# Kernel tuning notes

Measured on AMD Instinct MI355X. Metric: run time of the kernel, lower is better.

Reference implementation:

```python
import jax, jax.numpy as jnp
import numpy as np
import math

B, S, D, H, DK, DFF = 64, 512, 512, 8, 64, 2048


def _layernorm(x, g, b, eps=1e-5):
    mu = jnp.mean(x, axis=-1, keepdims=True)
    var = jnp.var(x, axis=-1, keepdims=True)
    return (x - mu) * jax.lax.rsqrt(var + eps) * g + b


def setup_inputs() -> dict:
    key = jax.random.key(0)
    ks = jax.random.split(key, 16)
    std = 0.02
    return {
        "query": jax.random.normal(ks[0], (B, S, D), jnp.float32),
        "key": jax.random.normal(ks[1], (B, S, D), jnp.float32),
        "values": jax.random.normal(ks[2], (B, S, D), jnp.float32),
        "forget_rate": jax.random.uniform(ks[3], (B, 1, S, 1), jnp.float32),
        "Wq": jax.random.normal(ks[4], (D, D), jnp.float32) * std,
        "bq": jnp.zeros((D,), jnp.float32),
        "Wk": jax.random.normal(ks[5], (D, D), jnp.float32) * std,
        "bk": jnp.zeros((D,), jnp.float32),
        "Wv": jax.random.normal(ks[6], (D, D), jnp.float32) * std,
        "bv": jnp.zeros((D,), jnp.float32),
        "Wo": jax.random.normal(ks[7], (D, D), jnp.float32) * std,
        "bo": jnp.zeros((D,), jnp.float32),
        "g1": jnp.ones((D,), jnp.float32),
        "beta1": jnp.zeros((D,), jnp.float32),
        "W1": jax.random.normal(ks[8], (D, DFF), jnp.float32) * std,
        "bf1": jnp.zeros((DFF,), jnp.float32),
        "W2": jax.random.normal(ks[9], (DFF, D), jnp.float32) * std,
        "bf2": jnp.zeros((D,), jnp.float32),
        "g2": jnp.ones((D,), jnp.float32),
        "beta2": jnp.zeros((D,), jnp.float32),
        "mask": 0,
    }


def reference(query, key, values, forget_rate, Wq, bq, Wk, bk, Wv, bv, Wo, bo,
              g1, beta1, W1, bf1, W2, bf2, g2, beta2, mask):
    bs, seqlen, _ = query.shape
    # project and split heads -> [B, H, S, DK]
    q = (query @ Wq + bq).reshape(bs, seqlen, H, DK).transpose(0, 2, 1, 3)
    k = (key @ Wk + bk).reshape(bs, seqlen, H, DK).transpose(0, 2, 1, 3)
    v = (values @ Wv + bv).reshape(bs, seqlen, H, DK).transpose(0, 2, 1, 3)

    scores = jnp.einsum('bhqd,bhkd->bhqk', q, k) / math.sqrt(DK)  # [B,H,S,S]
    # forget_rate [B,1,S,1] broadcasts over heads and key dim (== repeat in torch)
    scores = scores * forget_rate
    # src_mask: allowed where triu(ones, k=mask) == 0, i.e. j < i + mask
    allowed = jnp.tril(jnp.ones((seqlen, seqlen), bool), mask - 1)
    scores = jnp.where(allowed, scores, jnp.float32(-1e32))
    probs = jax.nn.softmax(scores, axis=-1)
    if mask == 0:  # zero_pad: overwrite first query row with zeros
        probs = probs.at[:, :, 0, :].set(0.0)
    out = jnp.einsum('bhqk,bhkd->bhqd', probs, v)  # [B,H,S,DK]
    concat = out.transpose(0, 2, 1, 3).reshape(bs, seqlen, D)
    attn_out = concat @ Wo + bo

    x = _layernorm(query + attn_out, g1, beta1)
    ff = jax.nn.relu(x @ W1 + bf1) @ W2 + bf2
    x = _layernorm(x + ff, g2, beta2)
    return x
```

## Files before the change

kernel.cpp:

```cpp
#include <hip/hip_runtime.h>
#include <hip/hip_bf16.h>
#include <stdint.h>

typedef __attribute__((ext_vector_type(8))) short short8;
typedef __attribute__((ext_vector_type(8))) unsigned short ushort8;
typedef __attribute__((ext_vector_type(4))) unsigned short ushort4v;
typedef __attribute__((ext_vector_type(4))) float f32x4;

#define DEV static __device__ __forceinline__

constexpr int Bc = 64, Sc = 512, Dc = 512, Hc = 8, DKc = 64, DFc = 2048;
constexpr int Mtot = Bc * Sc;
constexpr int CB   = 16;
constexpr int RC   = CB * Sc;
constexpr int RH   = 16384;

DEV unsigned short f2b(float f) {
    union { float f; unsigned u; } x; x.f = f;
    unsigned r = x.u + 0x7fffu + ((x.u >> 16) & 1u);
    return (unsigned short)(r >> 16);
}
DEV float b2f(unsigned short u) {
    union { unsigned u; float f; } x; x.u = ((unsigned)u) << 16; return x.f;
}

DEV void gload16(const void* g, void* l) {
    __builtin_amdgcn_global_load_lds(
        (const __attribute__((address_space(1))) void*)g,
        (__attribute__((address_space(3))) void*)l, 16, 0, 0);
}

__global__ void k_cvt(const float* __restrict__ in, unsigned short* __restrict__ out, int n8) {
    int idx = blockIdx.x * 256 + threadIdx.x;
    if (idx >= n8) return;
    const float4* p = (const float4*)(in + (size_t)idx * 8);
    float4 a = p[0], b = p[1];
    ushort8 o;
    o[0] = f2b(a.x); o[1] = f2b(a.y); o[2] = f2b(a.z); o[3] = f2b(a.w);
    o[4] = f2b(b.x); o[5] = f2b(b.y); o[6] = f2b(b.z); o[7] = f2b(b.w);
    *(ushort8*)(out + (size_t)idx * 8) = o;
}

__global__ void k_copy8(const unsigned short* __restrict__ in, unsigned short* __restrict__ out, int n8) {
    int idx = blockIdx.x * 256 + threadIdx.x;
    if (idx >= n8) return;
    *(ushort8*)(out + (size_t)idx * 8) = *(const ushort8*)(in + (size_t)idx * 8);
}

__global__ void k_cvt_w_all(
    const float* __restrict__ Wq, const float* __restrict__ Wk, const float* __restrict__ Wv,
    const float* __restrict__ Wo, const float* __restrict__ W1, const float* __restrict__ W2,
    unsigned short* __restrict__ Wqt, unsigned short* __restrict__ Wkt,
    unsigned short* __restrict__ Wvt, unsigned short* __restrict__ Wot,
    unsigned short* __restrict__ W1t, unsigned short* __restrict__ W2t) {
    int idx = blockIdx.x * 256 + threadIdx.x;
    const float* in; unsigned short* out; int K, N, li;
    if (idx < 131072) {
        int w = idx >> 15, r = idx & 32767;
        const float* ins[4] = {Wq, Wk, Wv, Wo};
        unsigned short* outs[4] = {Wqt, Wkt, Wvt, Wot};
        in = ins[w]; out = outs[w]; K = 512; N = 512; li = r;
    } else if (idx < 262144) {
        in = W1; out = W1t; K = 512; N = 2048; li = idx - 131072;
    } else {
        in = W2; out = W2t; K = 2048; N = 512; li = idx - 262144;
    }
    int kc = li % (K / 8), n = li / (K / 8);
    ushort8 o;
    #pragma unroll
    for (int j = 0; j < 8; ++j) o[j] = f2b(in[(size_t)(kc * 8 + j) * N + n]);
    *(ushort8*)(out + (size_t)n * K + kc * 8) = o;
}

template<int BM, int BN>
DEV void gemm_core(const unsigned short* __restrict__ A, int lda,
                   const unsigned short* __restrict__ Bt, int ldb, int K,
                   unsigned short* lA, unsigned short* lB,
                   f32x4 (&acc)[BM / 32][BN / 32]) {
    constexpr int MF = BM / 32, NF = BN / 32;
    const int tid = threadIdx.x, lane = tid & 63, wv = tid >> 6;
    const int wr = wv >> 1, wc = wv & 1;
    const int l15 = lane & 15, l4 = lane >> 4, l7 = l15 & 7;
    #pragma unroll
    for (int mf = 0; mf < MF; ++mf)
        #pragma unroll
        for (int nf = 0; nf < NF; ++nf)
            acc[mf][nf] = f32x4{0.f, 0.f, 0.f, 0.f};

    auto stage = [&](int buf, int kt0) {
        unsigned short* dA = lA + (size_t)buf * BM * 64;
        #pragma unroll
        for (int r = 0; r < BM / 32; ++r) {
            int c = r * 256 + tid, row = c >> 3, gs = c & 7;
            gload16(A + (size_t)row * lda + kt0 + ((gs ^ (row & 7)) * 8),
                    dA + (size_t)(r * 256 + wv * 64) * 8);
        }
        unsigned short* dB = lB + (size_t)buf * BN * 64;
        #pragma unroll
        for (int r = 0; r < BN / 32; ++r) {
            int c = r * 256 + tid, row = c >> 3, gs = c & 7;
            gload16(Bt + (size_t)row * ldb + kt0 + ((gs ^ (row & 7)) * 8),
                    dB + (size_t)(r * 256 + wv * 64) * 8);
        }
    };

    stage(0, 0);
    __syncthreads();
    const int nk = K / 64;
    for (int t = 0; t < nk; ++t) {
        const int buf = t & 1;
        if (t + 1 < nk) stage(buf ^ 1, (t + 1) * 64);
        const unsigned short* cA = lA + (size_t)buf * BM * 64;
        const unsigned short* cB = lB + (size_t)buf * BN * 64;
        #pragma unroll
        for (int kt = 0; kt < 2; ++kt) {
            short8 af[MF], bfr[NF];
            #pragma unroll
            for (int mf = 0; mf < MF; ++mf)
                af[mf] = *(const short8*)&cA[(wr * (BM / 2) + mf * 16 + l15) * 64 +
                                             (((kt * 4 + l4) ^ l7) * 8)];
            #pragma unroll
            for (int nf = 0; nf < NF; ++nf)
                bfr[nf] = *(const short8*)&cB[(wc * (BN / 2) + nf * 16 + l15) * 64 +
                                              (((kt * 4 + l4) ^ l7) * 8)];
            #pragma unroll
            for (int mf = 0; mf < MF; ++mf)
                #pragma unroll
                for (int nf = 0; nf < NF; ++nf)
                    acc[mf][nf] = __builtin_amdgcn_mfma_f32_16x16x32_bf16(af[mf], bfr[nf], acc[mf][nf], 0, 0, 0);
        }
        __syncthreads();
    }
}

__global__ __launch_bounds__(256) void k_gemm_qkv(
    const unsigned short* __restrict__ X, const unsigned short* __restrict__ Wt,
    const float* __restrict__ bias, unsigned short* __restrict__ out, int which) {
    __shared__ unsigned short lA[2 * 128 * 64], lB[2 * 128 * 64];
    int m0 = blockIdx.x * 128, n0 = blockIdx.y * 128;
    f32x4 acc[4][4];
    gemm_core<128, 128>(X + (size_t)m0 * Dc, Dc, Wt + (size_t)n0 * Dc, Dc, Dc, lA, lB, acc);
    const int lane = threadIdx.x & 63, wv = threadIdx.x >> 6;
    const int wr = wv >> 1, wc = wv & 1, l15 = lane & 15, l4 = lane >> 4;
    #pragma unroll
    for (int mf = 0; mf < 4; ++mf) {
        #pragma unroll
        for (int nf = 0; nf < 4; ++nf) {
            int n = n0 + wc * 64 + nf * 16 + l15;
            int h = n >> 6, dk = n & 63;
            float bv = bias[n];
            if (which == 2) {
                int mg = m0 + wr * 64 + mf * 16 + l4 * 4;
                int b = mg >> 9, s = mg & 511;
                ushort4v o;
                #pragma unroll
                for (int r = 0; r < 4; ++r) o[r] = f2b(acc[mf][nf][r] + bv);
                *(ushort4v*)&out[((size_t)(b * Hc + h) * DKc + dk) * Sc + s] = o;
            } else {
                float scale = (which == 0) ? 0.125f : 1.0f;
                #pragma unroll
                for (int r = 0; r < 4; ++r) {
                    int mg = m0 + wr * 64 + mf * 16 + l4 * 4 + r;
                    int b = mg >> 9, s = mg & 511;
                    out[((size_t)(b * Hc + h) * Sc + s) * DKc + dk] = f2b((acc[mf][nf][r] + bv) * scale);
                }
            }
        }
    }
}

__global__ __launch_bounds__(256) void k_flash(
    const unsigned short* __restrict__ Qb, const unsigned short* __restrict__ Kb,
    const unsigned short* __restrict__ Vt, unsigned short* __restrict__ conc,
    const float* __restrict__ fr, const int* __restrict__ maskp, int b_base) {
    __shared__ unsigned short lKb[2][64 * 64];
    __shared__ unsigned short lVb[2][64 * 64];
    __shared__ unsigned short lP[128 * 64];
    const int head = blockIdx.y, bl = head >> 3, h = head & 7;
    const int bg = b_base + bl;
    const int m0 = blockIdx.x * 128;
    const int mv = *maskp;
    const int tid = threadIdx.x, lane = tid & 63, w = tid >> 6;
    const int l15 = lane & 15, l4 = lane >> 4;
    const int l7 = l15 & 7;
    const int rw = w * 32;
    constexpr float LOG2E = 1.44269504088896340736f;

    unsigned short* lQ = &lKb[0][0];
    const unsigned short* Qg = Qb + ((size_t)head * Sc + m0) * DKc;
    #pragma unroll
    for (int r = 0; r < 4; ++r) {
        int c = r * 256 + tid, row = c >> 3, gs = c & 7;
        gload16(Qg + (size_t)row * DKc + ((gs ^ (row & 7)) * 8), lQ + (size_t)(r * 256 + w * 64) * 8);
    }
    __syncthreads();
    short8 qf[2][2];
    #pragma unroll
    for (int kt = 0; kt < 2; ++kt)
        #pragma unroll
        for (int mf = 0; mf < 2; ++mf)
            qf[kt][mf] = *(const short8*)&lQ[(rw + mf * 16 + l15) * 64 + (((kt * 4 + l4) ^ l7) * 8)];
    float frr[8];
    #pragma unroll
    for (int mf = 0; mf < 2; ++mf)
        #pragma unroll
        for (int r = 0; r < 4; ++r)
            frr[mf * 4 + r] = fr[(size_t)bg * Sc + m0 + rw + mf * 16 + l4 * 4 + r] * LOG2E;
    __syncthreads();

    f32x4 accO[2][4];
    #pragma unroll
    for (int mf = 0; mf < 2; ++mf)
        #pragma unroll
        for (int nf = 0; nf < 4; ++nf)
            accO[mf][nf] = f32x4{0.f, 0.f, 0.f, 0.f};
    float l_run[8];
    #pragma unroll
    for (int i = 0; i < 8; ++i) l_run[i] = 0.f;

    const unsigned short* Kg0 = Kb + (size_t)head * Sc * DKc;
    const unsigned short* Vg0 = Vt + (size_t)head * DKc * Sc;
    int nt = ((m0 + 126 + mv) >> 7) + 1;
    if (nt > 4) nt = 4;
    if (nt < 1) nt = 1;
    const int nc = nt * 2;

    {
        const unsigned short* Kg = Kg0;
        const unsigned short* Vg = Vg0;
        #pragma unroll
        for (int r = 0; r < 2; ++r) {
            int c = r * 256 + tid, row = c >> 3, gs = c & 7;
            gload16(Kg + (size_t)row * DKc + ((gs ^ (row & 7)) * 8), &lKb[0][0] + (size_t)(r * 256 + w * 64) * 8);
            gload16(Vg + (size_t)row * Sc + ((gs ^ (row & 7)) * 8), &lVb[0][0] + (size_t)(r * 256 + w * 64) * 8);
        }
    }
    __syncthreads();

    for (int ci = 0; ci < nc; ++ci) {
        const int buf = ci & 1;
        if (ci + 1 < nc) {
            int n1 = (ci + 1) * 64;
            const unsigned short* Kg = Kg0 + (size_t)n1 * DKc;
            const unsigned short* Vg = Vg0 + n1;
            #pragma unroll
            for (int r = 0; r < 2; ++r) {
                int c = r * 256 + tid, row = c >> 3, gs = c & 7;
                gload16(Kg + (size_t)row * DKc + ((gs ^ (row & 7)) * 8),
                        &lKb[buf ^ 1][0] + (size_t)(r * 256 + w * 64) * 8);
                gload16(Vg + (size_t)row * Sc + ((gs ^ (row & 7)) * 8),
                        &lVb[buf ^ 1][0] + (size_t)(r * 256 + w * 64) * 8);
            }
        }
        const int n0c = ci * 64;
        short8 bk[4][2];
        #pragma unroll
        for (int j = 0; j < 4; ++j)
            #pragma unroll
            for (int kt = 0; kt < 2; ++kt)
                bk[j][kt] = *(const short8*)&lKb[buf][(j * 16 + l15) * 64 + (((kt * 4 + l4) ^ l7) * 8)];
        #pragma unroll
        for (int mf = 0; mf < 2; ++mf) {
            f32x4 sa[4];
            #pragma unroll
            for (int j = 0; j < 4; ++j) sa[j] = f32x4{0.f, 0.f, 0.f, 0.f};
            #pragma unroll
            for (int kt = 0; kt < 2; ++kt)
                #pragma unroll
                for (int j = 0; j < 4; ++j)
                    sa[j] = __builtin_amdgcn_mfma_f32_16x16x32_bf16(qf[kt][mf], bk[j][kt], sa[j], 0, 0, 0);
            #pragma unroll
            for (int r = 0; r < 4; ++r) {
                int rowl = rw + mf * 16 + l4 * 4 + r;
                int rowg = m0 + rowl;
                int prs = rowl & 7;
                float fres = frr[mf * 4 + r];
                float ps = 0.f;
                #pragma unroll
                for (int j = 0; j < 4; ++j) {
                    int colg = n0c + j * 16 + l15;
                    float p = (colg < rowg + mv) ? exp2f(sa[j][r] * fres) : 0.f;
                    ps += p;
                    int gw = j * 2 + (l15 >> 3);
                    lP[rowl * 64 + ((gw ^ prs) * 8) + l7] = f2b(p);
                }
                l_run[mf * 4 + r] += ps;
            }
        }
        #pragma unroll
        for (int kl = 0; kl < 2; ++kl) {
            short8 pa[2];
            #pragma unroll
            for (int mf = 0; mf < 2; ++mf)
                pa[mf] = *(const short8*)&lP[(rw + mf * 16 + l15) * 64 + (((kl * 4 + l4) ^ l7) * 8)];
            #pragma unroll
            for (int nf = 0; nf < 4; ++nf) {
                short8 bv8 = *(const short8*)&lVb[buf][(nf * 16 + l15) * 64 + (((kl * 4 + l4) ^ l7) * 8)];
                #pragma unroll
                for (int mf = 0; mf < 2; ++mf)
                    accO[mf][nf] = __builtin_amdgcn_mfma_f32_16x16x32_bf16(pa[mf], bv8, accO[mf][nf], 0, 0, 0);
            }
        }
        __syncthreads();
    }
    #pragma unroll
    for (int mf = 0; mf < 2; ++mf)
        #pragma unroll
        for (int r = 0; r < 4; ++r) {
            int rowg = m0 + rw + mf * 16 + l4 * 4 + r;
            float l = l_run[mf * 4 + r];
            #pragma unroll
            for (int o = 1; o < 16; o <<= 1) l += __shfl_xor(l, o);
            float inv = (rowg + mv > 0) ? 1.0f / l : 0.f;
            #pragma unroll
            for (int nf = 0; nf < 4; ++nf) {
                int dk = nf * 16 + l15;
                conc[((size_t)bg * Sc + rowg) * Dc + h * DKc + dk] = f2b(accO[mf][nf][r] * inv);
            }
        }
}

__global__ __launch_bounds__(256) void k_wo(
    const unsigned short* __restrict__ Cc, const unsigned short* __restrict__ Wot,
    const float* __restrict__ bo, const float* __restrict__ query, float* __restrict__ y) {
    __shared__ unsigned short lA[2 * 128 * 64], lB[2 * 128 * 64];
    int m0 = blockIdx.x * 128, n0 = blockIdx.y * 128;
    f32x4 acc[4][4];
    gemm_core<128, 128>(Cc + (size_t)m0 * Dc, Dc, Wot + (size_t)n0 * Dc, Dc, Dc, lA, lB, acc);
    const int lane = threadIdx.x & 63, wv = threadIdx.x >> 6;
    const int wr = wv >> 1, wc = wv & 1, l15 = lane & 15, l4 = lane >> 4;
    #pragma unroll
    for (int mf = 0; mf < 4; ++mf)
        #pragma unroll
        for (int nf = 0; nf < 4; ++nf) {
            int n = n0 + wc * 64 + nf * 16 + l15;
            float bv = bo[n];
            #pragma unroll
            for (int r = 0; r < 4; ++r) {
                int m = m0 + wr * 64 + mf * 16 + l4 * 4 + r;
                y[(size_t)m * Dc + n] = acc[mf][nf][r] + bv + query[(size_t)m * Dc + n];
            }
        }
}

__global__ __launch_bounds__(256) void k_ff1(
    const unsigned short* __restrict__ X, const unsigned short* __restrict__ W1t,
    const float* __restrict__ b1, unsigned short* __restrict__ hb) {
    __shared__ unsigned short lA[2 * 128 * 64], lB[2 * 128 * 64];
    int m0 = blockIdx.x * 128, n0 = blockIdx.y * 128;
    f32x4 acc[4][4];
    gemm_core<128, 128>(X + (size_t)m0 * Dc, Dc, W1t + (size_t)n0 * Dc, Dc, Dc, lA, lB, acc);
    const int lane = threadIdx.x & 63, wv = threadIdx.x >> 6;
    const int wr = wv >> 1, wc = wv & 1, l15 = lane & 15, l4 = lane >> 4;
    #pragma unroll
    for (int mf = 0; mf < 4; ++mf)
        #pragma unroll
        for (int nf = 0; nf < 4; ++nf) {
            int n = n0 + wc * 64 + nf * 16 + l15;
            float bv = b1[n];
            #pragma unroll
            for (int r = 0; r < 4; ++r) {
                int m = m0 + wr * 64 + mf * 16 + l4 * 4 + r;
                hb[(size_t)m * DFc + n] = f2b(fmaxf(acc[mf][nf][r] + bv, 0.f));
            }
        }
}

__global__ __launch_bounds__(256) void k_ff2b(
    const unsigned short* __restrict__ Hb, const unsigned short* __restrict__ W2t,
    const float* __restrict__ b2, const unsigned short* __restrict__ residb,
    float* __restrict__ y) {
    __shared__ unsigned short lA[2 * 128 * 64], lB[2 * 128 * 64];
    int m0 = blockIdx.x * 128, n0 = blockIdx.y * 128;
    f32x4 acc[4][4];
    gemm_core<128, 128>(Hb + (size_t)m0 * DFc, DFc, W2t + (size_t)n0 * DFc, DFc, DFc, lA, lB, acc);
    const int lane = threadIdx.x & 63, wv = threadIdx.x >> 6;
    const int wr = wv >> 1, wc = wv & 1, l15 = lane & 15, l4 = lane >> 4;
    #pragma unroll
    for (int mf = 0; mf < 4; ++mf)
        #pragma unroll
        for (int nf = 0; nf < 4; ++nf) {
            int n = n0 + wc * 64 + nf * 16 + l15;
            float bv = b2[n];
            #pragma unroll
            for (int r = 0; r < 4; ++r) {
                int m = m0 + wr * 64 + mf * 16 + l4 * 4 + r;
                y[(size_t)m * Dc + n] = acc[mf][nf][r] + bv + b2f(residb[(size_t)m * Dc + n]);
            }
        }
}

__global__ __launch_bounds__(256) void k_ln(
    const float* __restrict__ in, const float* __restrict__ g, const float* __restrict__ be,
    float* __restrict__ outf, unsigned short* __restrict__ outb) {
    int rid = blockIdx.x * 4 + (threadIdx.x >> 6);
    int lane = threadIdx.x & 63;
    const float* row = in + (size_t)rid * Dc;
    float4 a = ((const float4*)row)[lane * 2];
    float4 b = ((const float4*)row)[lane * 2 + 1];
    float x[8] = {a.x, a.y, a.z, a.w, b.x, b.y, b.z, b.w};
    float s = 0.f, ss = 0.f;
    #pragma unroll
    for (int j = 0; j < 8; ++j) { s += x[j]; ss += x[j] * x[j]; }
    #pragma unroll
    for (int o = 1; o < 64; o <<= 1) { s += __shfl_xor(s, o); ss += __shfl_xor(ss, o); }
    float mu = s * (1.f / 512.f);
    float var = ss * (1.f / 512.f) - mu * mu;
    float rs = rsqrtf(var + 1e-5f);
    float4 g0 = ((const float4*)g)[lane * 2], g1v = ((const float4*)g)[lane * 2 + 1];
    float4 e0 = ((const float4*)be)[lane * 2], e1 = ((const float4*)be)[lane * 2 + 1];
    float gg[8] = {g0.x, g0.y, g0.z, g0.w, g1v.x, g1v.y, g1v.z, g1v.w};
    float ee[8] = {e0.x, e0.y, e0.z, e0.w, e1.x, e1.y, e1.z, e1.w};
    float o8[8];
    #pragma unroll
    for (int j = 0; j < 8; ++j) o8[j] = (x[j] - mu) * rs * gg[j] + ee[j];
    if (outf) {
        float4* po = (float4*)(outf + (size_t)rid * Dc);
        float4 w0 = {o8[0], o8[1], o8[2], o8[3]}, w1 = {o8[4], o8[5], o8[6], o8[7]};
        po[lane * 2] = w0; po[lane * 2 + 1] = w1;
    }
    if (outb) {
        ushort8 ob;
        #pragma unroll
        for (int j = 0; j < 8; ++j) ob[j] = f2b(o8[j]);
        *(ushort8*)(outb + (size_t)rid * Dc + lane * 8) = ob;
    }
}

extern "C" void kernel_launch(void* const* d_in, const int* in_sizes, int n_in,
                              void* d_out, int out_size, void* d_ws, size_t ws_size,
                              hipStream_t stream) {
    const float* query = (const float*)d_in[0];
    const float* key_  = (const float*)d_in[1];
    const float* vals  = (const float*)d_in[2];
    const float* fr    = (const float*)d_in[3];
    const float* Wq = (const float*)d_in[4];  const float* bq = (const float*)d_in[5];
    const float* Wk = (const float*)d_in[6];  const float* bk = (const float*)d_in[7];
    const float* Wv = (const float*)d_in[8];  const float* bv = (const float*)d_in[9];
    const float* Wo = (const float*)d_in[10]; const float* bo = (const float*)d_in[11];
    const float* g1 = (const float*)d_in[12]; const float* be1 = (const float*)d_in[13];
    const float* W1 = (const float*)d_in[14]; const float* b1 = (const float*)d_in[15];
    const float* W2 = (const float*)d_in[16]; const float* b2 = (const float*)d_in[17];
    const float* g2 = (const float*)d_in[18]; const float* be2 = (const float*)d_in[19];
    const int* maskp = (const int*)d_in[20];
    float* out = (float*)d_out;

    char* ab = (char*)d_out;
    unsigned short* xb   = (unsigned short*)ab;
    unsigned short* conc = (unsigned short*)ab;
    unsigned short* x1b  = conc;
    float*          xf   = (float*)(ab + (size_t)32 * 1048576);
    unsigned short* Qc   = (unsigned short*)(ab + (size_t)32 * 1048576);
    unsigned short* Kc   = (unsigned short*)(ab + (size_t)40 * 1048576);
    unsigned short* Vc   = (unsigned short*)(ab + (size_t)48 * 1048576);
    unsigned short* xst  = (unsigned short*)(ab + (size_t)56 * 1048576);

    char* ws = (char*)d_ws;
    unsigned short* Wqt = (unsigned short*)ws;
    unsigned short* Wkt = Wqt + 512 * 512;
    unsigned short* Wvt = Wkt + 512 * 512;
    unsigned short* Wot = Wvt + 512 * 512;
    unsigned short* W1t = Wot + 512 * 512;
    unsigned short* W2t = W1t + 2048 * 512;
    char* wend = (char*)(W2t + 512 * 2048);
    size_t wrem = (ws_size > (size_t)(wend - ws)) ? ws_size - (size_t)(wend - ws) : 0;
    const size_t qkvb = (size_t)Mtot * Dc * 2;

    bool bigpath = false;
    int Mc = 128;
    if (wrem >= 3 * qkvb + (size_t)128 * 5120) {
        bigpath = true;
        size_t rem2 = wrem - 3 * qkvb;
        for (int c = 8192; c >= 128; c >>= 1)
            if ((size_t)c * 5120 <= rem2) { Mc = c; break; }
    } else {
        for (int c = 8192; c >= 128; c >>= 1)
            if ((size_t)c * 5120 <= wrem) { Mc = c; break; }
    }
    unsigned short* hb     = (unsigned short*)wend;
    unsigned short* resid0 = (unsigned short*)(wend + (size_t)Mc * 4096);
    unsigned short* QbF    = (unsigned short*)(wend + (size_t)Mc * 5120);
    unsigned short* KbF    = QbF + qkvb / 2;
    unsigned short* VtF    = KbF + qkvb / 2;

    k_cvt_w_all<<<dim3(1536), dim3(256), 0, stream>>>(Wq, Wk, Wv, Wo, W1, W2,
                                                      Wqt, Wkt, Wvt, Wot, W1t, W2t);

    const float* acts[3] = {query, key_, vals};
    const unsigned short* wt3[3] = {Wqt, Wkt, Wvt};
    const float* bs3[3] = {bq, bk, bv};
    if (bigpath) {
        unsigned short* outF[3] = {QbF, KbF, VtF};
        for (int p = 0; p < 3; ++p) {
            k_cvt<<<dim3(Mtot * Dc / 8 / 256), dim3(256), 0, stream>>>(acts[p], xb, Mtot * Dc / 8);
            k_gemm_qkv<<<dim3(Mtot / 128, 4), dim3(256), 0, stream>>>(xb, wt3[p], bs3[p], outF[p], p);
        }
        k_flash<<<dim3(Sc / 128, Bc * Hc), dim3(256), 0, stream>>>(QbF, KbF, VtF, conc, fr, maskp, 0);
    } else {
        unsigned short* out3[3] = {Qc, Kc, Vc};
        for (int cb = 0; cb < Bc / CB; ++cb) {
            for (int p = 0; p < 3; ++p) {
                k_cvt<<<dim3(RC * Dc / 8 / 256), dim3(256), 0, stream>>>(
                    acts[p] + (size_t)cb * RC * Dc, xst, RC * Dc / 8);
                k_gemm_qkv<<<dim3(RC / 128, 4), dim3(256), 0, stream>>>(xst, wt3[p], bs3[p], out3[p], p);
            }
            k_flash<<<dim3(Sc / 128, CB * Hc), dim3(256), 0, stream>>>(Qc, Kc, Vc, conc, fr, maskp, cb * CB);
        }
    }

    for (int hp = 0; hp < 2; ++hp) {
        int mb = hp * RH;
        k_wo<<<dim3(RH / 128, 4), dim3(256), 0, stream>>>(conc + (size_t)mb * Dc, Wot, bo,
                                                          query + (size_t)mb * Dc, xf);
        k_ln<<<dim3(RH / 4), dim3(256), 0, stream>>>(xf, g1, be1, (float*)nullptr,
                                                     x1b + (size_t)mb * Dc);
    }

    k_copy8<<<dim3(Mc / 4), dim3(256), 0, stream>>>(x1b, resid0, Mc * Dc / 8);

    for (int mb = Mtot - Mc; mb >= 0; mb -= Mc) {
        k_ff1<<<dim3(Mc / 128, 16), dim3(256), 0, stream>>>(x1b + (size_t)mb * Dc, W1t, b1, hb);
        k_ff2b<<<dim3(Mc / 128, 4), dim3(256), 0, stream>>>(hb, W2t, b2,
                                                            mb ? x1b + (size_t)mb * Dc : resid0,
                                                            out + (size_t)mb * Dc);
        k_ln<<<dim3(Mc / 4), dim3(256), 0, stream>>>(out + (size_t)mb * Dc, g2, be2,
                                                     out + (size_t)mb * Dc, (unsigned short*)nullptr);
    }
}
```

Before: 667.9 us.

## Fuse weight and activation bf16 conversions into one launch and reuse buffers

```diff
diff --git a/kernel.cpp b/kernel.cpp
--- a/kernel.cpp
+++ b/kernel.cpp
@@ -13,7 +13,6 @@
 constexpr int Mtot = Bc * Sc;
 constexpr int CB   = 16;
 constexpr int RC   = CB * Sc;
-constexpr int RH   = 16384;
 
 DEV unsigned short f2b(float f) {
     union { float f; unsigned u; } x; x.f = f;
@@ -54,6 +53,48 @@
     unsigned short* __restrict__ Wvt, unsigned short* __restrict__ Wot,
     unsigned short* __restrict__ W1t, unsigned short* __restrict__ W2t) {
     int idx = blockIdx.x * 256 + threadIdx.x;
+    const float* in; unsigned short* out; int K, N, li;
+    if (idx < 131072) {
+        int w = idx >> 15, r = idx & 32767;
+        const float* ins[4] = {Wq, Wk, Wv, Wo};
+        unsigned short* outs[4] = {Wqt, Wkt, Wvt, Wot};
+        in = ins[w]; out = outs[w]; K = 512; N = 512; li = r;
+    } else if (idx < 262144) {
+        in = W1; out = W1t; K = 512; N = 2048; li = idx - 131072;
+    } else {
+        in = W2; out = W2t; K = 2048; N = 512; li = idx - 262144;
+    }
+    int kc = li % (K / 8), n = li / (K / 8);
+    ushort8 o;
+    #pragma unroll
+    for (int j = 0; j < 8; ++j) o[j] = f2b(in[(size_t)(kc * 8 + j) * N + n]);
+    *(ushort8*)(out + (size_t)n * K + kc * 8) = o;
+}
+
+__global__ void k_cvt_all(
+    const float* __restrict__ Wq, const float* __restrict__ Wk, const float* __restrict__ Wv,
+    const float* __restrict__ Wo, const float* __restrict__ W1, const float* __restrict__ W2,
+    unsigned short* __restrict__ Wqt, unsigned short* __restrict__ Wkt,
+    unsigned short* __restrict__ Wvt, unsigned short* __restrict__ Wot,
+    unsigned short* __restrict__ W1t, unsigned short* __restrict__ W2t,
+    const float* __restrict__ q_in, const float* __restrict__ k_in, const float* __restrict__ v_in,
+    unsigned short* __restrict__ q_out, unsigned short* __restrict__ k_out,
+    unsigned short* __restrict__ v_out) {
+    int idx = blockIdx.x * 256 + threadIdx.x;
+    if (idx >= 393216) {
+        int a = idx - 393216;
+        const float* in; unsigned short* out; int li;
+        if (a < 2097152)       { in = q_in; out = q_out; li = a; }
+        else if (a < 4194304)  { in = k_in; out = k_out; li = a - 2097152; }
+        else                   { in = v_in; out = v_out; li = a - 4194304; }
+        const float4* p = (const float4*)(in + (size_t)li * 8);
+        float4 x = p[0], y = p[1];
+        ushort8 o;
+        o[0] = f2b(x.x); o[1] = f2b(x.y); o[2] = f2b(x.z); o[3] = f2b(x.w);
+        o[4] = f2b(y.x); o[5] = f2b(y.y); o[6] = f2b(y.z); o[7] = f2b(y.w);
+        *(ushort8*)(out + (size_t)li * 8) = o;
+        return;
+    }
     const float* in; unsigned short* out; int K, N, li;
     if (idx < 131072) {
         int w = idx >> 15, r = idx & 32767;
@@ -446,14 +487,15 @@
     float* out = (float*)d_out;
 
     char* ab = (char*)d_out;
-    unsigned short* xb   = (unsigned short*)ab;
-    unsigned short* conc = (unsigned short*)ab;
-    unsigned short* x1b  = conc;
-    float*          xf   = (float*)(ab + (size_t)32 * 1048576);
+    unsigned short* xb    = (unsigned short*)ab;
+    unsigned short* conc  = (unsigned short*)ab;
+    unsigned short* x1b   = conc;
+    unsigned short* keyst = (unsigned short*)(ab + (size_t)32 * 1048576);
     unsigned short* Qc   = (unsigned short*)(ab + (size_t)32 * 1048576);
     unsigned short* Kc   = (unsigned short*)(ab + (size_t)40 * 1048576);
     unsigned short* Vc   = (unsigned short*)(ab + (size_t)48 * 1048576);
     unsigned short* xst  = (unsigned short*)(ab + (size_t)56 * 1048576);
+    float*          xfc  = (float*)(ab + (size_t)32 * 1048576);
 
     char* ws = (char*)d_ws;
     unsigned short* Wqt = (unsigned short*)ws;
@@ -466,37 +508,53 @@
     size_t wrem = (ws_size > (size_t)(wend - ws)) ? ws_size - (size_t)(wend - ws) : 0;
     const size_t qkvb = (size_t)Mtot * Dc * 2;
 
-    bool bigpath = false;
-    int Mc = 128;
-    if (wrem >= 3 * qkvb + (size_t)128 * 5120) {
-        bigpath = true;
-        size_t rem2 = wrem - 3 * qkvb;
-        for (int c = 8192; c >= 128; c >>= 1)
-            if ((size_t)c * 5120 <= rem2) { Mc = c; break; }
-    } else {
-        for (int c = 8192; c >= 128; c >>= 1)
-            if ((size_t)c * 5120 <= wrem) { Mc = c; break; }
-    }
-    unsigned short* hb     = (unsigned short*)wend;
-    unsigned short* resid0 = (unsigned short*)(wend + (size_t)Mc * 4096);
-    unsigned short* QbF    = (unsigned short*)(wend + (size_t)Mc * 5120);
-    unsigned short* KbF    = QbF + qkvb / 2;
-    unsigned short* VtF    = KbF + qkvb / 2;
-
-    k_cvt_w_all<<<dim3(1536), dim3(256), 0, stream>>>(Wq, Wk, Wv, Wo, W1, W2,
-                                                      Wqt, Wkt, Wvt, Wot, W1t, W2t);
+    const bool bigpath = (wrem >= 3 * qkvb);
 
     const float* acts[3] = {query, key_, vals};
     const unsigned short* wt3[3] = {Wqt, Wkt, Wvt};
     const float* bs3[3] = {bq, bk, bv};
+
     if (bigpath) {
-        unsigned short* outF[3] = {QbF, KbF, VtF};
-        for (int p = 0; p < 3; ++p) {
-            k_cvt<<<dim3(Mtot * Dc / 8 / 256), dim3(256), 0, stream>>>(acts[p], xb, Mtot * Dc / 8);
-            k_gemm_qkv<<<dim3(Mtot / 128, 4), dim3(256), 0, stream>>>(xb, wt3[p], bs3[p], outF[p], p);
-        }
+        unsigned short* QbF = (unsigned short*)wend;
+        unsigned short* KbF = QbF + qkvb / 2;
+        unsigned short* VtF = KbF + qkvb / 2;
+        unsigned short* hb     = QbF;
+        unsigned short* resid0 = VtF;
+        float*          xf     = (float*)KbF;
+        const int Mc = 16384;
+
+        k_cvt_all<<<dim3(26112), dim3(256), 0, stream>>>(
+            Wq, Wk, Wv, Wo, W1, W2, Wqt, Wkt, Wvt, Wot, W1t, W2t,
+            query, key_, vals, xb, keyst, KbF);
+
+        k_gemm_qkv<<<dim3(Mtot / 128, 4), dim3(256), 0, stream>>>(KbF,   Wvt, bv, VtF, 2);
+        k_gemm_qkv<<<dim3(Mtot / 128, 4), dim3(256), 0, stream>>>(keyst, Wkt, bk, KbF, 1);
+        k_gemm_qkv<<<dim3(Mtot / 128, 4), dim3(256), 0, stream>>>(xb,    Wqt, bq, QbF, 0);
+
         k_flash<<<dim3(Sc / 128, Bc * Hc), dim3(256), 0, stream>>>(QbF, KbF, VtF, conc, fr, maskp, 0);
+
+        k_wo<<<dim3(Mtot / 128, 4), dim3(256), 0, stream>>>(conc, Wot, bo, query, xf);
+        k_ln<<<dim3(Mtot / 4), dim3(256), 0, stream>>>(xf, g1, be1, (float*)nullptr, x1b);
+
+        k_copy8<<<dim3(Mc / 4), dim3(256), 0, stream>>>(x1b, resid0, Mc * Dc / 8);
+
+        for (int mb = Mtot - Mc; mb >= 0; mb -= Mc) {
+            k_ff1<<<dim3(Mc / 128, 16), dim3(256), 0, stream>>>(x1b + (size_t)mb * Dc, W1t, b1, hb);
+            k_ff2b<<<dim3(Mc / 128, 4), dim3(256), 0, stream>>>(hb, W2t, b2,
+                                                                mb ? x1b + (size_t)mb * Dc : resid0,
+                                                                out + (size_t)mb * Dc);
+            k_ln<<<dim3(Mc / 4), dim3(256), 0, stream>>>(out + (size_t)mb * Dc, g2, be2,
+                                                         out + (size_t)mb * Dc, (unsigned short*)nullptr);
+        }
     } else {
+        int Mc = 128;
+        for (int c = 8192; c >= 128; c >>= 1)
+            if ((size_t)c * 5120 <= wrem) { Mc = c; break; }
+        unsigned short* hb     = (unsigned short*)wend;
+        unsigned short* resid0 = (unsigned short*)(wend + (size_t)Mc * 4096);
+
+        k_cvt_w_all<<<dim3(1536), dim3(256), 0, stream>>>(Wq, Wk, Wv, Wo, W1, W2,
+                                                          Wqt, Wkt, Wvt, Wot, W1t, W2t);
         unsigned short* out3[3] = {Qc, Kc, Vc};
         for (int cb = 0; cb < Bc / CB; ++cb) {
             for (int p = 0; p < 3; ++p) {
@@ -506,24 +564,21 @@
             }
             k_flash<<<dim3(Sc / 128, CB * Hc), dim3(256), 0, stream>>>(Qc, Kc, Vc, conc, fr, maskp, cb * CB);
         }
-    }
-
-    for (int hp = 0; hp < 2; ++hp) {
-        int mb = hp * RH;
-        k_wo<<<dim3(RH / 128, 4), dim3(256), 0, stream>>>(conc + (size_t)mb * Dc, Wot, bo,
-                                                          query + (size_t)mb * Dc, xf);
-        k_ln<<<dim3(RH / 4), dim3(256), 0, stream>>>(xf, g1, be1, (float*)nullptr,
-                                                     x1b + (size_t)mb * Dc);
-    }
-
-    k_copy8<<<dim3(Mc / 4), dim3(256), 0, stream>>>(x1b, resid0, Mc * Dc / 8);
-
-    for (int mb = Mtot - Mc; mb >= 0; mb -= Mc) {
-        k_ff1<<<dim3(Mc / 128, 16), dim3(256), 0, stream>>>(x1b + (size_t)mb * Dc, W1t, b1, hb);
-        k_ff2b<<<dim3(Mc / 128, 4), dim3(256), 0, stream>>>(hb, W2t, b2,
-                                                            mb ? x1b + (size_t)mb * Dc : resid0,
-                                                            out + (size_t)mb * Dc);
-        k_ln<<<dim3(Mc / 4), dim3(256), 0, stream>>>(out + (size_t)mb * Dc, g2, be2,
-                                                     out + (size_t)mb * Dc, (unsigned short*)nullptr);
-    }
-}
+        for (int hp = 0; hp < 2; ++hp) {
+            int mb = hp * 16384;
+            k_wo<<<dim3(16384 / 128, 4), dim3(256), 0, stream>>>(conc + (size_t)mb * Dc, Wot, bo,
+                                                                 query + (size_t)mb * Dc, xfc);
+            k_ln<<<dim3(16384 / 4), dim3(256), 0, stream>>>(xfc, g1, be1, (float*)nullptr,
+                                                            x1b + (size_t)mb * Dc);
+        }
+        k_copy8<<<dim3(Mc / 4), dim3(256), 0, stream>>>(x1b, resid0, Mc * Dc / 8);
+        for (int mb = Mtot - Mc; mb >= 0; mb -= Mc) {
+            k_ff1<<<dim3(Mc / 128, 16), dim3(256), 0, stream>>>(x1b + (size_t)mb * Dc, W1t, b1, hb);
+            k_ff2b<<<dim3(Mc / 128, 4), dim3(256), 0, stream>>>(hb, W2t, b2,
+                                                                mb ? x1b + (size_t)mb * Dc : resid0,
+                                                                out + (size_t)mb * Dc);
+            k_ln<<<dim3(Mc / 4), dim3(256), 0, stream>>>(out + (size_t)mb * Dc, g2, be2,
+                                                         out + (size_t)mb * Dc, (unsigned short*)nullptr);
+        }
+    }
+}
```

Result: faster. 576.3 us (median of 2 runs) (-13.7%).
